# Kernel tuning notes

Measured on AMD Instinct MI355X. Metric: run time of the kernel, lower is better.

Reference implementation:

```python
import jax, jax.numpy as jnp
import numpy as np


def setup_inputs() -> dict:
    key = jax.random.key(0)
    ip = jax.random.normal(key, (8, 256, 128, 128), dtype=jnp.float32)
    return {"ip": ip}


def reference(ip):
    b, C, H, W = ip.shape
    two_c = 2 * C
    # precomputed complex shift grid: exp(-1j*2*pi*(C-0.5)*v/(2C)), v = 0..2C-1
    v = jnp.arange(two_c, dtype=jnp.float32)
    angle = -2.0 * jnp.pi * (C - 0.5) * v / two_c
    shift = (jnp.cos(angle) + 1j * jnp.sin(angle)).astype(jnp.complex64)  # [2C]

    viDct = ip * two_c                                   # [b, C, H, W]
    flip_neg = -viDct[:, 1:][:, ::-1]                    # [b, C-1, H, W]
    zeros = jnp.zeros((b, 1, H, W), dtype=ip.dtype)
    rev = jnp.concatenate([viDct, zeros, flip_neg], axis=1)  # [b, 2C, H, W]
    rev = rev.astype(jnp.complex64) * shift[None, :, None, None]
    vxx = jnp.fft.ifft(rev, axis=1)                      # norm='backward' (default)
    out = vxx[:, :C][:, ::-1].real                       # first C, flipped, real part
    return out.astype(ip.dtype)
```

## Files before the change

kernel.cpp:

```cpp
#include <hip/hip_runtime.h>
#include <hip/hip_bf16.h>
#include <math.h>

#define NB   8
#define NC   256
#define NHW  (128 * 128)

#define BN   64
#define BK   32
#define LSTR 80

typedef __attribute__((ext_vector_type(4))) float f32x4;
typedef __attribute__((ext_vector_type(8))) short bf16x8;

__device__ __forceinline__ unsigned f2bf_hi(float f) {
    unsigned u = __builtin_bit_cast(unsigned, f);
    u += 0x7fffu + ((u >> 16) & 1u);
    return u & 0xffff0000u;
}
__device__ __forceinline__ unsigned f2bf_lo(float f) {
    unsigned u = __builtin_bit_cast(unsigned, f);
    u += 0x7fffu + ((u >> 16) & 1u);
    return u >> 16;
}

__global__ void coef_kernel(unsigned short* __restrict__ coef) {
    int idx = blockIdx.x * 256 + threadIdx.x;
    int c = idx >> 8;
    int k = idx & 255;
    int t = (k * (2 * c + 1)) & 1023;
    float v = (k == 0) ? 1.0f : 2.0f * cosf((float)t * (float)(M_PI / 512.0));
    coef[idx] = (unsigned short)f2bf_lo(v);
}

__global__ __launch_bounds__(512, 4)
void dct_gemm(const float* __restrict__ X, const unsigned short* __restrict__ Mcoef,
              float* __restrict__ Out) {
    __shared__ unsigned char Xlds[2 * BN * LSTR];

    const int tid  = threadIdx.x;
    const int lane = tid & 63;
    const int wave = tid >> 6;
    const int wm   = wave >> 1;
    const int wn   = wave & 1;
    const int m16  = lane & 15;
    const int quad = lane >> 4;

    const int p0 = blockIdx.x * BN;
    const float* Xb = X + (size_t)blockIdx.y * (NC * NHW);
    float* Ob = Out + (size_t)blockIdx.y * (NC * NHW);

    const int sr = tid & 63;
    const int sh = tid >> 6;

    f32x4 acc[4][2];
#pragma unroll
    for (int i = 0; i < 4; i++)
#pragma unroll
        for (int j = 0; j < 2; j++) acc[i][j] = (f32x4){0.f, 0.f, 0.f, 0.f};

    const unsigned short* Abase = Mcoef + (wm * 64 + m16) * NC + quad * 8;
    const float* Xsrc0 = Xb + p0 + sr;

    float xv[4];
#pragma unroll
    for (int j = 0; j < 4; j++) xv[j] = Xsrc0[(sh * 4 + j) * NHW];
    bf16x8 afr[4];
#pragma unroll
    for (int mt = 0; mt < 4; mt++)
        afr[mt] = *(const bf16x8*)(Abase + mt * 16 * NC);

    for (int it = 0; it < NC / BK; ++it) {
        const int buf = (it & 1) * (BN * LSTR);

        {
            unsigned pk0 = f2bf_lo(xv[0]) | f2bf_hi(xv[1]);
            unsigned pk1 = f2bf_lo(xv[2]) | f2bf_hi(xv[3]);
            *(int2*)(Xlds + buf + sr * LSTR + sh * 8) = (int2){(int)pk0, (int)pk1};
        }
        __syncthreads();

        const int nk0 = ((it + 1) & (NC / BK - 1)) * BK;
        float xn[4];
#pragma unroll
        for (int j = 0; j < 4; j++) xn[j] = Xsrc0[(nk0 + sh * 4 + j) * NHW];
        bf16x8 an[4];
#pragma unroll
        for (int mt = 0; mt < 4; mt++)
            an[mt] = *(const bf16x8*)(Abase + mt * 16 * NC + nk0);

        bf16x8 bfr[2];
#pragma unroll
        for (int nt = 0; nt < 2; nt++) {
            int row = wn * 32 + nt * 16 + m16;
            bfr[nt] = *(const bf16x8*)(Xlds + buf + row * LSTR + quad * 16);
        }

#pragma unroll
        for (int mt = 0; mt < 4; mt++)
#pragma unroll
            for (int nt = 0; nt < 2; nt++)
                acc[mt][nt] = __builtin_amdgcn_mfma_f32_16x16x32_bf16(
                    afr[mt], bfr[nt], acc[mt][nt], 0, 0, 0);

#pragma unroll
        for (int j = 0; j < 4; j++) xv[j] = xn[j];
#pragma unroll
        for (int mt = 0; mt < 4; mt++) afr[mt] = an[mt];
    }

#pragma unroll
    for (int mt = 0; mt < 4; mt++) {
#pragma unroll
        for (int nt = 0; nt < 2; nt++) {
            int cc = wm * 64 + mt * 16 + quad * 4;
            int pp = p0 + wn * 32 + nt * 16 + m16;
            float* o = Ob + cc * NHW + pp;
#pragma unroll
            for (int r = 0; r < 4; r++)
                o[r * NHW] = acc[mt][nt][r];
        }
    }
}

extern "C" void kernel_launch(void* const* d_in, const int* in_sizes, int n_in,
                              void* d_out, int out_size, void* d_ws, size_t ws_size,
                              hipStream_t stream) {
    const float* ip = (const float*)d_in[0];
    float* out = (float*)d_out;
    unsigned short* coef = (unsigned short*)d_ws;

    coef_kernel<<<dim3(256), dim3(256), 0, stream>>>(coef);

    dim3 grid(NHW / BN, NB);
    dct_gemm<<<grid, dim3(512), 0, stream>>>(ip, coef, out);
}
```

Baseline: 260.0 us.

## Load whole K slab into swizzled LDS once, then run MFMA loop without syncs

Instead of streaming the 256-channel K dimension in 32-wide double-buffered steps with a barrier each step, each block now loads its full 64x256 bf16 tile of the input into LDS up front and issues one barrier. LDS rows are XOR-swizzled in 16-byte chunks to avoid bank conflicts, and the main loop is fully unrolled with only coefficient and LDS fragment loads. This removes the per-step synchronisation and gives each thread more loads in flight. The cost is a larger LDS footprint (32KB per block), which may limit occupancy, and no overlap between the global load phase and the MFMA phase.

```diff
diff --git a/kernel.cpp b/kernel.cpp
--- a/kernel.cpp
+++ b/kernel.cpp
@@ -6,22 +6,20 @@
 #define NC   256
 #define NHW  (128 * 128)
 
-#define BN   64
-#define BK   32
-#define LSTR 80
+#define BN 64
 
 typedef __attribute__((ext_vector_type(4))) float f32x4;
 typedef __attribute__((ext_vector_type(8))) short bf16x8;
 
+__device__ __forceinline__ unsigned f2bf_lo(float f) {
+    unsigned u = __builtin_bit_cast(unsigned, f);
+    u += 0x7fffu + ((u >> 16) & 1u);
+    return u >> 16;
+}
 __device__ __forceinline__ unsigned f2bf_hi(float f) {
     unsigned u = __builtin_bit_cast(unsigned, f);
     u += 0x7fffu + ((u >> 16) & 1u);
     return u & 0xffff0000u;
-}
-__device__ __forceinline__ unsigned f2bf_lo(float f) {
-    unsigned u = __builtin_bit_cast(unsigned, f);
-    u += 0x7fffu + ((u >> 16) & 1u);
-    return u >> 16;
 }
 
 __global__ void coef_kernel(unsigned short* __restrict__ coef) {
@@ -33,10 +31,14 @@
     coef[idx] = (unsigned short)f2bf_lo(v);
 }
 
+__device__ __forceinline__ int swz_off(int row, int chunk) {
+    return row * 512 + ((chunk ^ (row & 7)) << 4);
+}
+
 __global__ __launch_bounds__(512, 4)
 void dct_gemm(const float* __restrict__ X, const unsigned short* __restrict__ Mcoef,
               float* __restrict__ Out) {
-    __shared__ unsigned char Xlds[2 * BN * LSTR];
+    __shared__ unsigned char Xlds[BN * 512];
 
     const int tid  = threadIdx.x;
     const int lane = tid & 63;
@@ -52,6 +54,24 @@
 
     const int sr = tid & 63;
     const int sh = tid >> 6;
+    const float* xsrc = Xb + (size_t)(sh * 32) * NHW + p0 + sr;
+
+#pragma unroll
+    for (int half = 0; half < 2; ++half) {
+        float v[16];
+#pragma unroll
+        for (int j = 0; j < 16; j++) v[j] = xsrc[(half * 16 + j) * NHW];
+#pragma unroll
+        for (int cc = 0; cc < 2; cc++) {
+            int chunk = sh * 4 + half * 2 + cc;
+            int pk[4];
+#pragma unroll
+            for (int q = 0; q < 4; q++)
+                pk[q] = (int)(f2bf_lo(v[cc * 8 + 2 * q]) | f2bf_hi(v[cc * 8 + 2 * q + 1]));
+            *(int4*)(Xlds + swz_off(sr, chunk)) = (int4){pk[0], pk[1], pk[2], pk[3]};
+        }
+    }
+    __syncthreads();
 
     f32x4 acc[4][2];
 #pragma unroll
@@ -60,53 +80,23 @@
         for (int j = 0; j < 2; j++) acc[i][j] = (f32x4){0.f, 0.f, 0.f, 0.f};
 
     const unsigned short* Abase = Mcoef + (wm * 64 + m16) * NC + quad * 8;
-    const float* Xsrc0 = Xb + p0 + sr;
+    const int brow0 = wn * 32 + m16;
 
-    float xv[4];
 #pragma unroll
-    for (int j = 0; j < 4; j++) xv[j] = Xsrc0[(sh * 4 + j) * NHW];
-    bf16x8 afr[4];
-#pragma unroll
-    for (int mt = 0; mt < 4; mt++)
-        afr[mt] = *(const bf16x8*)(Abase + mt * 16 * NC);
-
-    for (int it = 0; it < NC / BK; ++it) {
-        const int buf = (it & 1) * (BN * LSTR);
-
-        {
-            unsigned pk0 = f2bf_lo(xv[0]) | f2bf_hi(xv[1]);
-            unsigned pk1 = f2bf_lo(xv[2]) | f2bf_hi(xv[3]);
-            *(int2*)(Xlds + buf + sr * LSTR + sh * 8) = (int2){(int)pk0, (int)pk1};
-        }
-        __syncthreads();
-
-        const int nk0 = ((it + 1) & (NC / BK - 1)) * BK;
-        float xn[4];
-#pragma unroll
-        for (int j = 0; j < 4; j++) xn[j] = Xsrc0[(nk0 + sh * 4 + j) * NHW];
-        bf16x8 an[4];
+    for (int s = 0; s < 8; ++s) {
+        bf16x8 afr[4], bfr[2];
 #pragma unroll
         for (int mt = 0; mt < 4; mt++)
-            an[mt] = *(const bf16x8*)(Abase + mt * 16 * NC + nk0);
-
-        bf16x8 bfr[2];
+            afr[mt] = *(const bf16x8*)(Abase + mt * 16 * NC + s * 32);
 #pragma unroll
-        for (int nt = 0; nt < 2; nt++) {
-            int row = wn * 32 + nt * 16 + m16;
-            bfr[nt] = *(const bf16x8*)(Xlds + buf + row * LSTR + quad * 16);
-        }
-
+        for (int nt = 0; nt < 2; nt++)
+            bfr[nt] = *(const bf16x8*)(Xlds + swz_off(brow0 + nt * 16, s * 4 + quad));
 #pragma unroll
         for (int mt = 0; mt < 4; mt++)
 #pragma unroll
             for (int nt = 0; nt < 2; nt++)
                 acc[mt][nt] = __builtin_amdgcn_mfma_f32_16x16x32_bf16(
                     afr[mt], bfr[nt], acc[mt][nt], 0, 0, 0);
-
-#pragma unroll
-        for (int j = 0; j < 4; j++) xv[j] = xn[j];
-#pragma unroll
-        for (int mt = 0; mt < 4; mt++) afr[mt] = an[mt];
     }
 
 #pragma unroll
```

Result: slower. 268.7 us (+3.4%).

## Drop LDS staging; load X fragments directly into registers per wave

Applied to the files above, without the earlier changes.

The GEMM no longer stages X through a double-buffered shared-memory tile with barriers. Each lane now loads its B fragment straight from global memory, converts it to bf16 in registers and feeds the MFMA. The block shrinks to 4 waves covering 32 pixels, the K loop is fully unrolled, and strided output indexing switches to size_t. This removes LDS traffic and __syncthreads. The cost is more scattered global loads (16-float segments per row stride), more register use, and X reads duplicated across the four waves of a block.

```diff
diff --git a/kernel.cpp b/kernel.cpp
--- a/kernel.cpp
+++ b/kernel.cpp
@@ -6,22 +6,18 @@
 #define NC   256
 #define NHW  (128 * 128)
 
-#define BN   64
-#define BK   32
-#define LSTR 80
-
 typedef __attribute__((ext_vector_type(4))) float f32x4;
 typedef __attribute__((ext_vector_type(8))) short bf16x8;
 
+__device__ __forceinline__ unsigned f2bf_lo(float f) {
+    unsigned u = __builtin_bit_cast(unsigned, f);
+    u += 0x7fffu + ((u >> 16) & 1u);
+    return u >> 16;
+}
 __device__ __forceinline__ unsigned f2bf_hi(float f) {
     unsigned u = __builtin_bit_cast(unsigned, f);
     u += 0x7fffu + ((u >> 16) & 1u);
     return u & 0xffff0000u;
-}
-__device__ __forceinline__ unsigned f2bf_lo(float f) {
-    unsigned u = __builtin_bit_cast(unsigned, f);
-    u += 0x7fffu + ((u >> 16) & 1u);
-    return u >> 16;
 }
 
 __global__ void coef_kernel(unsigned short* __restrict__ coef) {
@@ -33,25 +29,21 @@
     coef[idx] = (unsigned short)f2bf_lo(v);
 }
 
-__global__ __launch_bounds__(512, 4)
+__global__ __launch_bounds__(256, 4)
 void dct_gemm(const float* __restrict__ X, const unsigned short* __restrict__ Mcoef,
               float* __restrict__ Out) {
-    __shared__ unsigned char Xlds[2 * BN * LSTR];
-
     const int tid  = threadIdx.x;
     const int lane = tid & 63;
-    const int wave = tid >> 6;
-    const int wm   = wave >> 1;
-    const int wn   = wave & 1;
+    const int wm   = tid >> 6;
     const int m16  = lane & 15;
     const int quad = lane >> 4;
 
-    const int p0 = blockIdx.x * BN;
+    const int p0 = blockIdx.x * 32;
     const float* Xb = X + (size_t)blockIdx.y * (NC * NHW);
     float* Ob = Out + (size_t)blockIdx.y * (NC * NHW);
 
-    const int sr = tid & 63;
-    const int sh = tid >> 6;
+    const float* xlane = Xb + (size_t)(quad * 8) * NHW + p0 + m16;
+    const unsigned short* Abase = Mcoef + (wm * 64 + m16) * NC + quad * 8;
 
     f32x4 acc[4][2];
 #pragma unroll
@@ -59,41 +51,40 @@
 #pragma unroll
         for (int j = 0; j < 2; j++) acc[i][j] = (f32x4){0.f, 0.f, 0.f, 0.f};
 
-    const unsigned short* Abase = Mcoef + (wm * 64 + m16) * NC + quad * 8;
-    const float* Xsrc0 = Xb + p0 + sr;
-
-    float xv[4];
+    float bv[2][8];
+    bf16x8 afr[4];
 #pragma unroll
-    for (int j = 0; j < 4; j++) xv[j] = Xsrc0[(sh * 4 + j) * NHW];
-    bf16x8 afr[4];
+    for (int nt = 0; nt < 2; nt++)
+#pragma unroll
+        for (int j = 0; j < 8; j++) bv[nt][j] = xlane[j * NHW + nt * 16];
 #pragma unroll
     for (int mt = 0; mt < 4; mt++)
         afr[mt] = *(const bf16x8*)(Abase + mt * 16 * NC);
 
-    for (int it = 0; it < NC / BK; ++it) {
-        const int buf = (it & 1) * (BN * LSTR);
-
-        {
-            unsigned pk0 = f2bf_lo(xv[0]) | f2bf_hi(xv[1]);
-            unsigned pk1 = f2bf_lo(xv[2]) | f2bf_hi(xv[3]);
-            *(int2*)(Xlds + buf + sr * LSTR + sh * 8) = (int2){(int)pk0, (int)pk1};
+#pragma unroll
+    for (int s = 0; s < 8; ++s) {
+        float bn[2][8];
+        bf16x8 an[4];
+        if (s < 7) {
+            const int k1 = (s + 1) * 32;
+#pragma unroll
+            for (int nt = 0; nt < 2; nt++)
+#pragma unroll
+                for (int j = 0; j < 8; j++) bn[nt][j] = xlane[(k1 + j) * NHW + nt * 16];
+#pragma unroll
+            for (int mt = 0; mt < 4; mt++)
+                an[mt] = *(const bf16x8*)(Abase + mt * 16 * NC + k1);
         }
-        __syncthreads();
-
-        const int nk0 = ((it + 1) & (NC / BK - 1)) * BK;
-        float xn[4];
-#pragma unroll
-        for (int j = 0; j < 4; j++) xn[j] = Xsrc0[(nk0 + sh * 4 + j) * NHW];
-        bf16x8 an[4];
-#pragma unroll
-        for (int mt = 0; mt < 4; mt++)
-            an[mt] = *(const bf16x8*)(Abase + mt * 16 * NC + nk0);
 
         bf16x8 bfr[2];
 #pragma unroll
         for (int nt = 0; nt < 2; nt++) {
-            int row = wn * 32 + nt * 16 + m16;
-            bfr[nt] = *(const bf16x8*)(Xlds + buf + row * LSTR + quad * 16);
+            int4 pk;
+            pk.x = (int)(f2bf_lo(bv[nt][0]) | f2bf_hi(bv[nt][1]));
+            pk.y = (int)(f2bf_lo(bv[nt][2]) | f2bf_hi(bv[nt][3]));
+            pk.z = (int)(f2bf_lo(bv[nt][4]) | f2bf_hi(bv[nt][5]));
+            pk.w = (int)(f2bf_lo(bv[nt][6]) | f2bf_hi(bv[nt][7]));
+            bfr[nt] = __builtin_bit_cast(bf16x8, pk);
         }
 
 #pragma unroll
@@ -103,10 +94,14 @@
                 acc[mt][nt] = __builtin_amdgcn_mfma_f32_16x16x32_bf16(
                     afr[mt], bfr[nt], acc[mt][nt], 0, 0, 0);
 
+        if (s < 7) {
 #pragma unroll
-        for (int j = 0; j < 4; j++) xv[j] = xn[j];
+            for (int nt = 0; nt < 2; nt++)
 #pragma unroll
-        for (int mt = 0; mt < 4; mt++) afr[mt] = an[mt];
+                for (int j = 0; j < 8; j++) bv[nt][j] = bn[nt][j];
+#pragma unroll
+            for (int mt = 0; mt < 4; mt++) afr[mt] = an[mt];
+        }
     }
 
 #pragma unroll
@@ -114,11 +109,11 @@
 #pragma unroll
         for (int nt = 0; nt < 2; nt++) {
             int cc = wm * 64 + mt * 16 + quad * 4;
-            int pp = p0 + wn * 32 + nt * 16 + m16;
-            float* o = Ob + cc * NHW + pp;
+            int pp = p0 + nt * 16 + m16;
+            float* o = Ob + (size_t)cc * NHW + pp;
 #pragma unroll
             for (int r = 0; r < 4; r++)
-                o[r * NHW] = acc[mt][nt][r];
+                o[(size_t)r * NHW] = acc[mt][nt][r];
         }
     }
 }
@@ -132,6 +127,6 @@
 
     coef_kernel<<<dim3(256), dim3(256), 0, stream>>>(coef);
 
-    dim3 grid(NHW / BN, NB);
-    dct_gemm<<<grid, dim3(512), 0, stream>>>(ip, coef, out);
+    dim3 grid(NHW / 32, NB);
+    dct_gemm<<<grid, dim3(256), 0, stream>>>(ip, coef, out);
 }
```

Result: slower. 309.4 us (+19.0%).
